# Kernel tuning notes

Measured on AMD Instinct MI355X. Metric: run time of the kernel, lower is better.

## Reference

```python
import jax, jax.numpy as jnp
import numpy as np

N, D_MODEL, D_DICT, K = 8192, 2048, 16384, 64


def setup_inputs() -> dict:
    key = jax.random.key(0)
    k1, k2, k3 = jax.random.split(key, 3)
    x = jax.random.normal(k1, (N, D_MODEL), dtype=jnp.float32)
    # xavier-uniform-like init for encoder weight (d_dict, d_model)
    limit = float(np.sqrt(6.0 / (D_MODEL + D_DICT)))
    W_enc_w = jax.random.uniform(k2, (D_DICT, D_MODEL), dtype=jnp.float32,
                                 minval=-limit, maxval=limit)
    b_enc = jnp.zeros((D_DICT,), dtype=jnp.float32)
    # decoder initialized as W_enc^T with unit-norm columns
    W_dec_w = W_enc_w.T  # (d_model, d_dict)
    norms = jnp.clip(jnp.linalg.norm(W_dec_w, axis=0, keepdims=True), 1e-8)
    W_dec_w = W_dec_w / norms
    b_dec = jnp.zeros((D_MODEL,), dtype=jnp.float32)
    return {"x": x, "W_enc_w": W_enc_w, "b_enc": b_enc,
            "W_dec_w": W_dec_w, "b_dec": b_dec, "k": K}


def reference(x, W_enc_w, b_enc, W_dec_w, b_dec, k):
    # encode: relu of linear on bias-centered input
    x_centered = x - b_dec                                   # [N, d_model]
    pre_acts = jax.nn.relu(x_centered @ W_enc_w.T + b_enc)   # [N, d_dict]
    # top-k select + scatter back to sparse dense vector
    topk_vals, topk_idx = jax.lax.top_k(pre_acts, k)         # [N, k]
    rows = jnp.arange(pre_acts.shape[0])[:, None]
    h = jnp.zeros_like(pre_acts).at[rows, topk_idx].set(topk_vals)
    # decode
    x_hat = h @ W_dec_w.T + b_dec                            # [N, d_model]
    # metrics
    recon_loss = jnp.mean((x_hat - x) ** 2)
    l0 = jnp.mean(jnp.sum(h > 0, axis=-1).astype(x.dtype))
    total_var = jnp.sum((x - jnp.mean(x, axis=0, keepdims=True)) ** 2)
    residual_var = jnp.sum((x - x_hat) ** 2)
    explained_var = 1.0 - residual_var / (total_var + 1e-8)
    return x_hat, h, recon_loss, l0, explained_var
```

## Files before the change

### kernel.cpp

```cpp
#include <hip/hip_runtime.h>
#include <hip/hip_bf16.h>
#include <stdint.h>

#define AS1 __attribute__((address_space(1)))
#define AS3 __attribute__((address_space(3)))

using bf16x8 = __attribute__((ext_vector_type(8))) short;
using f32x4  = __attribute__((ext_vector_type(4))) float;

static constexpr int NROWS = 8192;
static constexpr int DM    = 2048;
static constexpr int DD    = 16384;
static constexpr int KSEL  = 64;
static constexpr int CCAP  = 768;
static constexpr int SLOTS = 24;
static constexpr int SORTN = 256;
#define POOLTHR 1.0f
#define MARGIN  0.03f

using OutT = unsigned short;

__device__ __forceinline__ unsigned short f2bf(float f) {
  unsigned u = __float_as_uint(f);
  u += 0x7FFFu + ((u >> 16) & 1u);
  return (unsigned short)(u >> 16);
}
__device__ __forceinline__ void gload16(const void* g, void* l) {
  __builtin_amdgcn_global_load_lds((const AS1 void*)g, (AS3 void*)l, 16, 0, 0);
}

__global__ void k_init(double* __restrict__ colsum, unsigned* __restrict__ rowcnt) {
  if (blockIdx.x == 0) {
    for (int i = threadIdx.x; i < 2048 + 8; i += 256) colsum[i] = 0.0;
  } else {
    rowcnt[(blockIdx.x - 1) * 256 + threadIdx.x] = 0u;
  }
}

__global__ void k_convx_stats(const float* __restrict__ x, const float* __restrict__ bd,
                              OutT* __restrict__ xb, double* __restrict__ colsum,
                              double* __restrict__ accs) {
  __shared__ double rd[256];
  const int b = blockIdx.x;
  const int c0 = threadIdx.x * 8;
  float4 bv0 = *(const float4*)(bd + c0);
  float4 bv1 = *(const float4*)(bd + c0 + 4);
  float s0=0,s1=0,s2=0,s3=0,s4=0,s5=0,s6=0,s7=0;
  double sq = 0.0;
  for (int r = 0; r < 128; ++r) {
    const size_t base = (size_t)(b * 128 + r) * DM + c0;
    float4 u = *(const float4*)(x + base);
    float4 v = *(const float4*)(x + base + 4);
    s0+=u.x; s1+=u.y; s2+=u.z; s3+=u.w; s4+=v.x; s5+=v.y; s6+=v.z; s7+=v.w;
    sq += (double)u.x*u.x + (double)u.y*u.y + (double)u.z*u.z + (double)u.w*u.w
        + (double)v.x*v.x + (double)v.y*v.y + (double)v.z*v.z + (double)v.w*v.w;
    unsigned o0 = f2bf(u.x - bv0.x), o1 = f2bf(u.y - bv0.y);
    unsigned o2 = f2bf(u.z - bv0.z), o3 = f2bf(u.w - bv0.w);
    unsigned o4 = f2bf(v.x - bv1.x), o5 = f2bf(v.y - bv1.y);
    unsigned o6 = f2bf(v.z - bv1.z), o7 = f2bf(v.w - bv1.w);
    uint4 p;
    p.x = o0 | (o1 << 16); p.y = o2 | (o3 << 16);
    p.z = o4 | (o5 << 16); p.w = o6 | (o7 << 16);
    *(uint4*)(xb + base) = p;
  }
  atomicAdd(&colsum[c0+0], (double)s0); atomicAdd(&colsum[c0+1], (double)s1);
  atomicAdd(&colsum[c0+2], (double)s2); atomicAdd(&colsum[c0+3], (double)s3);
  atomicAdd(&colsum[c0+4], (double)s4); atomicAdd(&colsum[c0+5], (double)s5);
  atomicAdd(&colsum[c0+6], (double)s6); atomicAdd(&colsum[c0+7], (double)s7);
  rd[threadIdx.x] = sq; __syncthreads();
  for (int off = 128; off > 0; off >>= 1) {
    if ((int)threadIdx.x < off) rd[threadIdx.x] += rd[threadIdx.x + off];
    __syncthreads();
  }
  if (threadIdx.x == 0) atomicAdd(&accs[2], rd[0]);
}

__global__ void k_conv_w(const float* __restrict__ src, OutT* __restrict__ dst) {
  size_t i = ((size_t)blockIdx.x * blockDim.x + threadIdx.x) * 8;
  float4 a = *(const float4*)(src + i);
  float4 b = *(const float4*)(src + i + 4);
  unsigned o0 = f2bf(a.x), o1 = f2bf(a.y), o2 = f2bf(a.z), o3 = f2bf(a.w);
  unsigned o4 = f2bf(b.x), o5 = f2bf(b.y), o6 = f2bf(b.z), o7 = f2bf(b.w);
  uint4 p;
  p.x = o0 | (o1 << 16); p.y = o2 | (o3 << 16);
  p.z = o4 | (o5 << 16); p.w = o6 | (o7 << 16);
  *(uint4*)(dst + i) = p;
}

__global__ void k_twdec(const float* __restrict__ wd, OutT* __restrict__ wdt) {
  __shared__ float t[32][33];
  const int ct = blockIdx.x;
  const int rt = blockIdx.y;
  const int tid = threadIdx.x;
  const int r  = tid >> 3;
  const int c4 = (tid & 7) * 4;
  float4 v = *(const float4*)(wd + (size_t)(rt * 32 + r) * DD + ct * 32 + c4);
  t[r][c4 + 0] = v.x; t[r][c4 + 1] = v.y; t[r][c4 + 2] = v.z; t[r][c4 + 3] = v.w;
  __syncthreads();
  unsigned a = f2bf(t[c4 + 0][r]), b = f2bf(t[c4 + 1][r]);
  unsigned c = f2bf(t[c4 + 2][r]), d = f2bf(t[c4 + 3][r]);
  uint2 p; p.x = a | (b << 16); p.y = c | (d << 16);
  *(uint2*)(wdt + (size_t)(ct * 32 + r) * DM + rt * 32 + c4) = p;
}

__global__ __launch_bounds__(256, 2) void k_gemm(
    const OutT* __restrict__ A,
    const OutT* __restrict__ B,
    const float* __restrict__ bias,
    float* __restrict__ h,
    unsigned* __restrict__ poolc,
    unsigned* __restrict__ rowcnt)
{
  __shared__ __align__(16) unsigned smem[4096];
  OutT* As = (OutT*)smem;
  OutT* Bs = (OutT*)smem + 4096;
  unsigned (*lpool)[SLOTS] = (unsigned(*)[SLOTS])smem;
  unsigned* lcnt  = smem + 128 * SLOTS;
  unsigned* lbase = smem + 128 * SLOTS + 128;

  const int bid = blockIdx.x;
  const int xcd = bid & 7;
  const int idx = bid >> 3;
  const int bn  = xcd * 16 + (idx & 15);
  const int bm  = idx >> 4;
  const int tid = threadIdx.x;
  const int lane = tid & 63;
  const int wv = tid >> 6;
  const int wm = wv >> 1, wn = wv & 1;

  const int c0 = wv * 2, c1 = wv * 2 + 1;
  const int sr0 = c0 * 16 + (lane >> 2);
  const int sr1 = c1 * 16 + (lane >> 2);
  const int sk  = (lane & 3) * 8;
  const OutT* gA0 = A + (size_t)(bm * 128 + sr0) * DM + sk;
  const OutT* gA1 = A + (size_t)(bm * 128 + sr1) * DM + sk;
  const OutT* gB0 = B + (size_t)(bn * 128 + sr0) * DM + sk;
  const OutT* gB1 = B + (size_t)(bn * 128 + sr1) * DM + sk;
  OutT* lA0 = &As[c0 * 512];
  OutT* lA1 = &As[c1 * 512];
  OutT* lB0 = &Bs[c0 * 512];
  OutT* lB1 = &Bs[c1 * 512];

  const int fr = lane & 15;
  const int kg = (lane >> 4) * 8;

  f32x4 acc[4][4] = {};

  for (int kt = 0; kt < DM / 32; ++kt) {
    gload16(gA0, lA0); gload16(gA1, lA1);
    gload16(gB0, lB0); gload16(gB1, lB1);
    gA0 += 32; gA1 += 32; gB0 += 32; gB1 += 32;
    __syncthreads();
    bf16x8 af[4], bfr[4];
#pragma unroll
    for (int m = 0; m < 4; ++m)
      af[m] = *(const bf16x8*)&As[(wm * 64 + m * 16 + fr) * 32 + kg];
#pragma unroll
    for (int n = 0; n < 4; ++n)
      bfr[n] = *(const bf16x8*)&Bs[(wn * 64 + n * 16 + fr) * 32 + kg];
#pragma unroll
    for (int m = 0; m < 4; ++m)
#pragma unroll
      for (int n = 0; n < 4; ++n)
        acc[m][n] = __builtin_amdgcn_mfma_f32_16x16x32_bf16(af[m], bfr[n], acc[m][n], 0, 0, 0);
    __syncthreads();
  }

  if (tid < 128) lcnt[tid] = 0;
  __syncthreads();
  const int r0 = (lane >> 4) * 4;
#pragma unroll
  for (int n = 0; n < 4; ++n) {
    const int col = bn * 128 + wn * 64 + n * 16 + fr;
    const float bv = bias[col];
#pragma unroll
    for (int m = 0; m < 4; ++m) {
      const int lr = wm * 64 + m * 16 + r0;
#pragma unroll
      for (int r = 0; r < 4; ++r) {
        float v = acc[m][n][r] + bv;
        if (v > POOLTHR) {
          unsigned pos = atomicAdd(&lcnt[lr + r], 1u);
          if (pos < (unsigned)SLOTS)
            lpool[lr + r][pos] = ((unsigned)f2bf(v) << 16) | (unsigned)col;
        }
      }
    }
  }
  __syncthreads();
  if (tid < 128) {
    unsigned c = lcnt[tid]; if (c > (unsigned)SLOTS) c = SLOTS;
    lcnt[tid] = c;
    lbase[tid] = c ? atomicAdd(&rowcnt[bm * 128 + tid], c) : 0u;
  }
  __syncthreads();
  for (int i = tid; i < 128 * SLOTS; i += 256) {
    const int lr = i / SLOTS;
    const int slot = i - lr * SLOTS;
    if (slot < (int)lcnt[lr]) {
      unsigned p = lbase[lr] + (unsigned)slot;
      if (p < (unsigned)CCAP)
        poolc[(size_t)(bm * 128 + lr) * CCAP + p] = lpool[lr][slot];
    }
  }
  const f32x4 z4 = {0.f, 0.f, 0.f, 0.f};
  for (int i = tid; i < 4096; i += 256) {
    const int lr = i >> 5, cc = i & 31;
    __builtin_nontemporal_store(z4,
        (f32x4*)(h + (size_t)(bm * 128 + lr) * DD + bn * 128) + cc);
  }
}

__global__ __launch_bounds__(256) void k_select(
    unsigned* __restrict__ hbuf,
    const unsigned* __restrict__ poolc,
    const unsigned* __restrict__ rowcnt,
    const float* __restrict__ x,
    const float* __restrict__ bd,
    const float* __restrict__ wenc,
    const float* __restrict__ benc,
    double* __restrict__ accs)
{
  __shared__ float xls[DM];
  __shared__ unsigned hist[256];
  __shared__ unsigned spool[CCAP];
  __shared__ int   cidx[SORTN];
  __shared__ float cval[SORTN];
  __shared__ unsigned long long skey[SORTN];
  __shared__ int   snc, snk;
  __shared__ float sthr;

  const int row  = blockIdx.x;
  const int tid  = threadIdx.x;
  const int lane = tid & 63;
  const int wid  = tid >> 6;
  const float* xr = x + (size_t)row * DM;
  unsigned cnt = rowcnt[row]; if (cnt > (unsigned)CCAP) cnt = CCAP;

  for (int i = tid; i < DM / 4; i += 256) {
    f32x4 xv = __builtin_nontemporal_load((const f32x4*)xr + i);
    f32x4 bv = ((const f32x4*)bd)[i];
    ((f32x4*)xls)[i] = xv - bv;
  }
  hist[tid] = 0;
  if (tid == 0) snc = 0;
  __syncthreads();

  f32x4 xreg[8];
#pragma unroll
  for (int t = 0; t < 8; ++t)
    xreg[t] = ((const f32x4*)xls)[t * 64 + lane];

  const unsigned* prow = poolc + (size_t)row * CCAP;
  for (int i = tid; i < (int)cnt; i += 256) {
    unsigned p = __builtin_nontemporal_load(prow + i);
    spool[i] = p;
    float v = __uint_as_float(p & 0xFFFF0000u);
    int b = (int)(v * 128.f); if (b > 255) b = 255;
    atomicAdd(&hist[b], 1u);
  }
  __syncthreads();
  if (tid == 0) {
    unsigned cum = 0; int b = 255; bool found = false;
    for (; b >= 128; --b) {
      cum += hist[b];
      if (cum >= (unsigned)KSEL) { found = true; break; }
    }
    sthr = found ? ((float)b * 0.0078125f - MARGIN) : 0.99f;
  }
  __syncthreads();
  const float thr = sthr;

  for (int i = tid; i < (int)cnt; i += 256) {
    unsigned p = spool[i];
    float v = __uint_as_float(p & 0xFFFF0000u);
    if (v > thr) { int q = atomicAdd(&snc, 1); if (q < SORTN) cidx[q] = (int)(p & 0xFFFFu); }
  }
  __syncthreads();
  const int NC = snc < SORTN ? snc : SORTN;

  for (int c = wid; c < NC; c += 4) {
    const float* wr = wenc + (size_t)cidx[c] * DM;
    f32x4 p = {0.f, 0.f, 0.f, 0.f};
#pragma unroll
    for (int t = 0; t < 8; ++t) {
      f32x4 w4 = *(const f32x4*)(wr + t * 256 + lane * 4);
      p[0] = fmaf(xreg[t][0], w4[0], p[0]);
      p[1] = fmaf(xreg[t][1], w4[1], p[1]);
      p[2] = fmaf(xreg[t][2], w4[2], p[2]);
      p[3] = fmaf(xreg[t][3], w4[3], p[3]);
    }
    float s = (p[0] + p[1]) + (p[2] + p[3]);
#pragma unroll
    for (int off = 1; off < 64; off <<= 1)
      s += __shfl_xor(s, off);
    if (lane == 0) cval[c] = s + benc[cidx[c]];
  }
  __syncthreads();

  {
    unsigned long long k = 0ULL;
    if (tid < NC) {
      float pv = cval[tid];
      if (pv > 0.f)
        k = ((unsigned long long)__float_as_uint(pv) << 32)
          | (unsigned)(DD - 1 - cidx[tid]);
    }
    skey[tid] = k;
  }
  __syncthreads();

  for (int k = 2; k <= SORTN; k <<= 1) {
    for (int j = k >> 1; j > 0; j >>= 1) {
      int ixj = tid ^ j;
      if (ixj > tid) {
        unsigned long long a = skey[tid], b = skey[ixj];
        bool blockUp = (tid & k) == 0;
        if (blockUp ? (a < b) : (a > b)) { skey[tid] = b; skey[ixj] = a; }
      }
      __syncthreads();
    }
  }

  if (tid == 0) {
    int c = 0;
    for (int j = 0; j < KSEL; ++j) c += (skey[j] != 0ULL) ? 1 : 0;
    snk = c;
    atomicAdd(&accs[1], (double)c);
  }
  __syncthreads();
  const int nk = snk;

  if (tid < KSEL) {
    unsigned long long k = skey[tid];
    uint2 s;
    if (tid < nk) {
      s.x = (unsigned)((DD - 1) - (int)(k & 0xFFFFFFFFu));
      s.y = (unsigned)(k >> 32);
    } else {
      s.x = 0xFFFFFFFFu;
      s.y = 0u;
    }
    ((uint2*)(hbuf + (size_t)row * 16384))[tid] = s;
  }
}

__global__ __launch_bounds__(256) void k_finish(
    float* __restrict__ h,
    const OutT* __restrict__ wdt,
    const float* __restrict__ x,
    const float* __restrict__ bd,
    float* __restrict__ xhat,
    double* __restrict__ accs)
{
  __shared__ int   sidx[KSEL];
  __shared__ float sval[KSEL];
  __shared__ float red[256];

  const int row = blockIdx.x;
  const int tid = threadIdx.x;
  float* hrow = h + (size_t)row * DD;

  if (tid < KSEL) {
    uint2 p = ((const uint2*)hrow)[tid];
    sidx[tid] = (int)p.x;
    sval[tid] = __uint_as_float(p.y);
  }
  __syncthreads();
  if (tid < KSEL) ((float2*)hrow)[tid] = make_float2(0.f, 0.f);
  __syncthreads();
  if (tid < KSEL && sidx[tid] >= 0) hrow[sidx[tid]] = sval[tid];

  const int d0 = tid * 8;
  f32x4 bv0 = ((const f32x4*)bd)[tid * 2];
  f32x4 bv1 = ((const f32x4*)bd)[tid * 2 + 1];
  float a0=bv0[0], a1=bv0[1], a2=bv0[2], a3=bv0[3];
  float a4=bv1[0], a5=bv1[1], a6=bv1[2], a7=bv1[3];
  for (int j = 0; j < KSEL; ++j) {
    if (sidx[j] < 0) continue;
    const float vv = sval[j];
    const uint4 w = *(const uint4*)(wdt + (size_t)sidx[j] * DM + d0);
    a0 = fmaf(vv, __uint_as_float(w.x << 16), a0);
    a1 = fmaf(vv, __uint_as_float(w.x & 0xFFFF0000u), a1);
    a2 = fmaf(vv, __uint_as_float(w.y << 16), a2);
    a3 = fmaf(vv, __uint_as_float(w.y & 0xFFFF0000u), a3);
    a4 = fmaf(vv, __uint_as_float(w.z << 16), a4);
    a5 = fmaf(vv, __uint_as_float(w.z & 0xFFFF0000u), a5);
    a6 = fmaf(vv, __uint_as_float(w.w << 16), a6);
    a7 = fmaf(vv, __uint_as_float(w.w & 0xFFFF0000u), a7);
  }
  const float* xr = x + (size_t)row * DM + d0;
  f32x4 xv0 = __builtin_nontemporal_load((const f32x4*)xr);
  f32x4 xv1 = __builtin_nontemporal_load((const f32x4*)(xr + 4));
  float s = 0.f, d;
  d = a0 - xv0[0]; s += d*d; d = a1 - xv0[1]; s += d*d;
  d = a2 - xv0[2]; s += d*d; d = a3 - xv0[3]; s += d*d;
  d = a4 - xv1[0]; s += d*d; d = a5 - xv1[1]; s += d*d;
  d = a6 - xv1[2]; s += d*d; d = a7 - xv1[3]; s += d*d;
  f32x4 o0 = {a0, a1, a2, a3};
  f32x4 o1 = {a4, a5, a6, a7};
  float* xo = xhat + (size_t)row * DM + d0;
  __builtin_nontemporal_store(o0, (f32x4*)xo);
  __builtin_nontemporal_store(o1, (f32x4*)(xo + 4));

  red[tid] = s; __syncthreads();
  for (int off = 128; off > 0; off >>= 1) {
    if (tid < off) red[tid] += red[tid + off];
    __syncthreads();
  }
  if (tid == 0) atomicAdd(&accs[0], (double)red[0]);
}

__global__ void k_final(const double* __restrict__ colsum, const double* __restrict__ accs,
                        float* __restrict__ osc) {
  __shared__ double rd[256];
  double s = 0.0;
  for (int c = threadIdx.x; c < DM; c += 256) { double m = colsum[c]; s += m * m; }
  rd[threadIdx.x] = s; __syncthreads();
  for (int off = 128; off > 0; off >>= 1) {
    if ((int)threadIdx.x < off) rd[threadIdx.x] += rd[threadIdx.x + off];
    __syncthreads();
  }
  if (threadIdx.x == 0) {
    double res = accs[0];
    double tv  = accs[2] - rd[0] / (double)NROWS;
    osc[0] = (float)(res / ((double)NROWS * (double)DM));
    osc[1] = (float)(accs[1] / (double)NROWS);
    osc[2] = (float)(1.0 - res / (tv + 1e-8));
  }
}

extern "C" void kernel_launch(void* const* d_in, const int* in_sizes, int n_in,
                              void* d_out, int out_size, void* d_ws, size_t ws_size,
                              hipStream_t stream) {
  (void)in_sizes; (void)n_in; (void)out_size; (void)ws_size;
  const float* x    = (const float*)d_in[0];
  const float* wenc = (const float*)d_in[1];
  const float* benc = (const float*)d_in[2];
  const float* wdec = (const float*)d_in[3];
  const float* bdec = (const float*)d_in[4];

  float* out  = (float*)d_out;
  float* xhat = out;
  float* hbuf = out + (size_t)NROWS * DM;
  float* osc  = out + (size_t)NROWS * DM + (size_t)NROWS * DD;

  OutT*     xb      = (OutT*)d_out;
  unsigned* xs32    = (unsigned*)d_out;
  unsigned* poolc   = xs32 + (size_t)8 * 1024 * 1024;
  unsigned* rowcnt  = poolc + (size_t)NROWS * CCAP;

  char* w = (char*)d_ws;
  OutT*   web    = (OutT*)w;
  OutT*   wdt    = (OutT*)(w + 67108864);
  double* colsum = (double*)(w + 134217728);
  double* accs   = (double*)(w + 134217728 + 16384);

  k_init       <<<1 + NROWS / 256, 256, 0, stream>>>(colsum, rowcnt);
  k_convx_stats<<<NROWS / 128, 256, 0, stream>>>(x, bdec, xb, colsum, accs);
  k_conv_w     <<<(DD * DM) / (256 * 8), 256, 0, stream>>>(wenc, web);
  k_gemm       <<<(NROWS / 128) * (DD / 128), 256, 0, stream>>>(xb, web, benc, hbuf, poolc, rowcnt);
  k_select     <<<NROWS, 256, 0, stream>>>((unsigned*)hbuf, poolc, rowcnt, x, bdec, wenc, benc, accs);
  k_twdec      <<<dim3(DD / 32, DM / 32), 256, 0, stream>>>(wdec, wdt);
  k_finish     <<<NROWS, 256, 0, stream>>>(hbuf, wdt, x, bdec, xhat, accs);
  k_final      <<<1, 256, 0, stream>>>(colsum, accs, osc);
}
```

Before: 1.837 ms.

## Rescore top-k candidates with fp16 weights, refine boundary ones in fp32

Adds an fp16 copy of the encoder weights. The select kernel now scores candidate features against that copy, halving the bytes gathered per candidate. Candidates whose score lies within a small delta of the 64th value are then recomputed in fp32, and the list is sorted again before the final top-k. This costs an extra conversion kernel, an extra bitonic sort and a refinement pass, and exact selection now depends on the delta being wide enough to cover fp16 error.

```diff
diff --git a/kernel.cpp b/kernel.cpp
--- a/kernel.cpp
+++ b/kernel.cpp
@@ -7,6 +7,8 @@
 
 using bf16x8 = __attribute__((ext_vector_type(8))) short;
 using f32x4  = __attribute__((ext_vector_type(4))) float;
+using f16x4  = __attribute__((ext_vector_type(4))) _Float16;
+using f16x8  = __attribute__((ext_vector_type(8))) _Float16;
 
 static constexpr int NROWS = 8192;
 static constexpr int DM    = 2048;
@@ -15,8 +17,10 @@
 static constexpr int CCAP  = 768;
 static constexpr int SLOTS = 24;
 static constexpr int SORTN = 256;
+static constexpr int BCAP  = 64;
 #define POOLTHR 1.0f
 #define MARGIN  0.03f
+#define DELTA   1.0e-3f
 
 using OutT = unsigned short;
 
@@ -87,6 +91,16 @@
   *(uint4*)(dst + i) = p;
 }
 
+__global__ void k_conv_h(const float* __restrict__ src, _Float16* __restrict__ dst) {
+  size_t i = ((size_t)blockIdx.x * blockDim.x + threadIdx.x) * 8;
+  float4 a = *(const float4*)(src + i);
+  float4 b = *(const float4*)(src + i + 4);
+  f16x8 o;
+  o[0] = (_Float16)a.x; o[1] = (_Float16)a.y; o[2] = (_Float16)a.z; o[3] = (_Float16)a.w;
+  o[4] = (_Float16)b.x; o[5] = (_Float16)b.y; o[6] = (_Float16)b.z; o[7] = (_Float16)b.w;
+  *(f16x8*)(dst + i) = o;
+}
+
 __global__ void k_twdec(const float* __restrict__ wd, OutT* __restrict__ wdt) {
   __shared__ float t[32][33];
   const int ct = blockIdx.x;
@@ -218,6 +232,7 @@
     const float* __restrict__ x,
     const float* __restrict__ bd,
     const float* __restrict__ wenc,
+    const _Float16* __restrict__ wh,
     const float* __restrict__ benc,
     double* __restrict__ accs)
 {
@@ -227,7 +242,8 @@
   __shared__ int   cidx[SORTN];
   __shared__ float cval[SORTN];
   __shared__ unsigned long long skey[SORTN];
-  __shared__ int   snc, snk;
+  __shared__ int   bidx[BCAP];
+  __shared__ int   snc, snk, sbc;
   __shared__ float sthr;
 
   const int row  = blockIdx.x;
@@ -243,7 +259,7 @@
     ((f32x4*)xls)[i] = xv - bv;
   }
   hist[tid] = 0;
-  if (tid == 0) snc = 0;
+  if (tid == 0) { snc = 0; sbc = 0; }
   __syncthreads();
 
   f32x4 xreg[8];
@@ -280,15 +296,15 @@
   const int NC = snc < SORTN ? snc : SORTN;
 
   for (int c = wid; c < NC; c += 4) {
-    const float* wr = wenc + (size_t)cidx[c] * DM;
+    const _Float16* wr = wh + (size_t)cidx[c] * DM;
     f32x4 p = {0.f, 0.f, 0.f, 0.f};
 #pragma unroll
     for (int t = 0; t < 8; ++t) {
-      f32x4 w4 = *(const f32x4*)(wr + t * 256 + lane * 4);
-      p[0] = fmaf(xreg[t][0], w4[0], p[0]);
-      p[1] = fmaf(xreg[t][1], w4[1], p[1]);
-      p[2] = fmaf(xreg[t][2], w4[2], p[2]);
-      p[3] = fmaf(xreg[t][3], w4[3], p[3]);
+      f16x4 wq = *(const f16x4*)(wr + t * 256 + lane * 4);
+      p[0] = fmaf(xreg[t][0], (float)wq[0], p[0]);
+      p[1] = fmaf(xreg[t][1], (float)wq[1], p[1]);
+      p[2] = fmaf(xreg[t][2], (float)wq[2], p[2]);
+      p[3] = fmaf(xreg[t][3], (float)wq[3], p[3]);
     }
     float s = (p[0] + p[1]) + (p[2] + p[3]);
 #pragma unroll
@@ -309,7 +325,66 @@
     skey[tid] = k;
   }
   __syncthreads();
-
+  for (int k = 2; k <= SORTN; k <<= 1) {
+    for (int j = k >> 1; j > 0; j >>= 1) {
+      int ixj = tid ^ j;
+      if (ixj > tid) {
+        unsigned long long a = skey[tid], b = skey[ixj];
+        bool blockUp = (tid & k) == 0;
+        if (blockUp ? (a < b) : (a > b)) { skey[tid] = b; skey[ixj] = a; }
+      }
+      __syncthreads();
+    }
+  }
+  float v64a = 0.f;
+  {
+    unsigned long long kk = skey[KSEL - 1];
+    if (kk != 0ULL) v64a = __uint_as_float((unsigned)(kk >> 32));
+    else {
+      for (int j = KSEL - 1; j >= 0; --j)
+        if (skey[j] != 0ULL) { v64a = __uint_as_float((unsigned)(skey[j] >> 32)); break; }
+    }
+  }
+
+  for (int i = tid; i < NC; i += 256) {
+    if (fabsf(cval[i] - v64a) <= DELTA) {
+      int q = atomicAdd(&sbc, 1);
+      if (q < BCAP) bidx[q] = i;
+    }
+  }
+  __syncthreads();
+  const int nb = sbc < BCAP ? sbc : BCAP;
+  for (int b2 = wid; b2 < nb; b2 += 4) {
+    const int c = bidx[b2];
+    const float* wr = wenc + (size_t)cidx[c] * DM;
+    f32x4 p = {0.f, 0.f, 0.f, 0.f};
+#pragma unroll
+    for (int t = 0; t < 8; ++t) {
+      f32x4 w4 = *(const f32x4*)(wr + t * 256 + lane * 4);
+      p[0] = fmaf(xreg[t][0], w4[0], p[0]);
+      p[1] = fmaf(xreg[t][1], w4[1], p[1]);
+      p[2] = fmaf(xreg[t][2], w4[2], p[2]);
+      p[3] = fmaf(xreg[t][3], w4[3], p[3]);
+    }
+    float s = (p[0] + p[1]) + (p[2] + p[3]);
+#pragma unroll
+    for (int off = 1; off < 64; off <<= 1)
+      s += __shfl_xor(s, off);
+    if (lane == 0) cval[c] = s + benc[cidx[c]];
+  }
+  __syncthreads();
+
+  {
+    unsigned long long k = 0ULL;
+    if (tid < NC) {
+      float pv = cval[tid];
+      if (pv > 0.f)
+        k = ((unsigned long long)__float_as_uint(pv) << 32)
+          | (unsigned)(DD - 1 - cidx[tid]);
+    }
+    skey[tid] = k;
+  }
+  __syncthreads();
   for (int k = 2; k <= SORTN; k <<= 1) {
     for (int j = k >> 1; j > 0; j >>= 1) {
       int ixj = tid ^ j;
@@ -451,7 +526,8 @@
   unsigned* rowcnt  = poolc + (size_t)NROWS * CCAP;
 
   char* w = (char*)d_ws;
-  OutT*   web    = (OutT*)w;
+  OutT*      web    = (OutT*)w;
+  _Float16*  wh     = (_Float16*)w;
   OutT*   wdt    = (OutT*)(w + 67108864);
   double* colsum = (double*)(w + 134217728);
   double* accs   = (double*)(w + 134217728 + 16384);
@@ -460,7 +536,8 @@
   k_convx_stats<<<NROWS / 128, 256, 0, stream>>>(x, bdec, xb, colsum, accs);
   k_conv_w     <<<(DD * DM) / (256 * 8), 256, 0, stream>>>(wenc, web);
   k_gemm       <<<(NROWS / 128) * (DD / 128), 256, 0, stream>>>(xb, web, benc, hbuf, poolc, rowcnt);
-  k_select     <<<NROWS, 256, 0, stream>>>((unsigned*)hbuf, poolc, rowcnt, x, bdec, wenc, benc, accs);
+  k_conv_h     <<<(DD * DM) / (256 * 8), 256, 0, stream>>>(wenc, wh);
+  k_select     <<<NROWS, 256, 0, stream>>>((unsigned*)hbuf, poolc, rowcnt, x, bdec, wenc, wh, benc, accs);
   k_twdec      <<<dim3(DD / 32, DM / 32), 256, 0, stream>>>(wdec, wdt);
   k_finish     <<<NROWS, 256, 0, stream>>>(hbuf, wdt, x, bdec, xhat, accs);
   k_final      <<<1, 256, 0, stream>>>(colsum, accs, osc);
```

After: 1.554 ms. 1.18x faster.
